# Kernel tuning notes

Measured on AMD Instinct MI355X. Metric: run time of the kernel, lower is better.

Reference implementation:

```python
import jax, jax.numpy as jnp
import numpy as np

EMB = 1024
HID = 4096
B = 2
T = 4096
NUM_BLOCK = 24
EPS = 1e-6


def rmsnorm(x):
    # unparameterized RMS normalization over last dim
    return x * jax.lax.rsqrt(jnp.mean(jnp.square(x), axis=-1, keepdims=True) + EPS)


def setup_inputs() -> dict:
    key = jax.random.key(0)
    k1, k2, k3, k4 = jax.random.split(key, 4)
    x = jax.random.normal(k1, (B, T, EMB), dtype=jnp.float32)
    W1 = 0.02 * jax.random.normal(k2, (HID, EMB), dtype=jnp.float32)
    W2 = 0.02 * jax.random.normal(k3, (HID, EMB), dtype=jnp.float32)
    W3 = (0.02 / np.sqrt(NUM_BLOCK)) * jax.random.normal(k4, (EMB, HID), dtype=jnp.float32)
    return {"x": x, "W1": W1, "W2": W2, "W3": W3}


def bar_quadratic_causal_preact_stable(a, b):
    # y_t = (1/t^2) * sum_{i<=t} sum_{j<=t} exp(a_i + b_j), per feature channel.
    # exp factorizes, so compute stably via log-cumsum-exp along the seq axis.
    seq = a.shape[1]
    log_t = jnp.log(jnp.arange(1, seq + 1, dtype=a.dtype))  # [T]
    la = jax.lax.cumlogsumexp(a, axis=1)  # [B,T,H]
    lb = jax.lax.cumlogsumexp(b, axis=1)  # [B,T,H]
    return jnp.exp(la + lb - 2.0 * log_t[None, :, None])


def reference(x, W1, W2, W3):
    r = rmsnorm(x)
    a = jnp.einsum('bte,he->bth', r, W1)  # fc_1, no bias
    b = jnp.einsum('bte,he->bth', r, W2)  # fc_2, no bias
    r = bar_quadratic_causal_preact_stable(a, b)
    r = rmsnorm(r)
    r = jnp.einsum('bth,eh->bte', r, W3)  # fc_3, no bias
    return x + r
```

## Files before the change

kernel.cpp:

```cpp
#include <hip/hip_runtime.h>
#include <hip/hip_fp8.h>

#define EMB 1024
#define HID 4096
#define NB 2
#define TT 4096
#define MROWS (NB*TT)
#define N1 (2*HID)
#define CHUNK 128
#define NCH 32

typedef short short8 __attribute__((ext_vector_type(8)));
typedef float v4f   __attribute__((ext_vector_type(4)));
typedef int   v4i   __attribute__((ext_vector_type(4)));
typedef int   v8i   __attribute__((ext_vector_type(8)));

__device__ __forceinline__ unsigned short f2bf(float f) {
  unsigned int u = __float_as_uint(f);
  u += 0x7FFFu + ((u >> 16) & 1u);
  return (unsigned short)(u >> 16);
}
__device__ __forceinline__ float bf2f(unsigned short s) {
  return __uint_as_float(((unsigned int)s) << 16);
}
__device__ __forceinline__ unsigned char f2e4m3(float f) {
  __hip_fp8_e4m3 q(f);
  return *(unsigned char*)&q;
}
__device__ __forceinline__ float e4m32f(unsigned char c) {
  __hip_fp8_e4m3 q = *(__hip_fp8_e4m3*)&c;
  return (float)q;
}
__device__ __forceinline__ void g2l16(const void* g, void* l) {
  __builtin_amdgcn_global_load_lds(
      (const __attribute__((address_space(1))) void*)g,
      (__attribute__((address_space(3))) void*)l, 16, 0, 0);
}

__device__ __forceinline__ float block_reduce_sum(float v, float* sbuf) {
  #pragma unroll
  for (int off = 32; off; off >>= 1) v += __shfl_down(v, off, 64);
  int lane = threadIdx.x & 63, w = threadIdx.x >> 6;
  if (lane == 0) sbuf[w] = v;
  __syncthreads();
  return sbuf[0] + sbuf[1] + sbuf[2] + sbuf[3];
}

__global__ __launch_bounds__(256) void conv_all(const float* __restrict__ W1,
                                                const float* __restrict__ W2,
                                                const float* __restrict__ W3,
                                                unsigned short* __restrict__ o12,
                                                unsigned char* __restrict__ o3) {
  size_t i = ((size_t)blockIdx.x*256 + threadIdx.x)*4;
  if (i < 2ull*HID*EMB) {
    const float* s = (i < (size_t)HID*EMB) ? (W1 + i) : (W2 + (i - (size_t)HID*EMB));
    float4 v = *(const float4*)s;
    ushort4 u; u.x=f2bf(v.x); u.y=f2bf(v.y); u.z=f2bf(v.z); u.w=f2bf(v.w);
    *(ushort4*)(o12 + i) = u;
  } else {
    size_t off = i - 2ull*HID*EMB;
    float4 v = *(const float4*)(W3 + off);
    uchar4 u; u.x=f2e4m3(v.x*64.f); u.y=f2e4m3(v.y*64.f);
             u.z=f2e4m3(v.z*64.f); u.w=f2e4m3(v.w*64.f);
    *(uchar4*)(o3 + off) = u;
  }
}

__global__ __launch_bounds__(256) void rmsnorm_x(const float* __restrict__ x,
                                                 unsigned short* __restrict__ r) {
  __shared__ float sbuf[4];
  int row = blockIdx.x;
  float4 v = *(const float4*)(x + (size_t)row*EMB + threadIdx.x*4);
  float ss = v.x*v.x + v.y*v.y + v.z*v.z + v.w*v.w;
  float tot = block_reduce_sum(ss, sbuf);
  float sc = rsqrtf(tot * (1.0f/EMB) + 1e-6f);
  ushort4 o; o.x=f2bf(v.x*sc); o.y=f2bf(v.y*sc); o.z=f2bf(v.z*sc); o.w=f2bf(v.w*sc);
  *(ushort4*)(r + (size_t)row*EMB + threadIdx.x*4) = o;
}

__global__ __launch_bounds__(256, 2)
void gemm_exp(const unsigned short* __restrict__ A,
              const unsigned short* __restrict__ Bt,
              unsigned char* __restrict__ C8,
              float* __restrict__ part,
              int K, int N) {
  __shared__ short lA[128*64];
  __shared__ short lB[128*64];
  const int tid  = threadIdx.x;
  const int lane = tid & 63;
  const int wm   = (tid >> 6) >> 1, wn = (tid >> 6) & 1;
  const int bid  = blockIdx.x;
  const int s0i  = bid >> 3;
  const int rowTile = s0i >> 3;
  const int colTile = ((bid & 7) << 3) | (s0i & 7);
  const int rowBase = rowTile * 128;
  const int colBase = colTile * 128;

  v4f acc[4][4];
  #pragma unroll
  for (int i=0;i<4;++i)
    #pragma unroll
    for (int j=0;j<4;++j) acc[i][j] = (v4f){0.f,0.f,0.f,0.f};

  for (int k0 = 0; k0 < K; k0 += 64) {
    #pragma unroll
    for (int j = 0; j < 4; ++j) {
      int s = j*256 + tid;
      int m = s >> 3;
      int c = (s & 7) ^ (m & 7);
      g2l16(A + (size_t)(rowBase + m)*K + k0 + c*8, &lA[s*8]);
    }
    #pragma unroll
    for (int j = 0; j < 4; ++j) {
      int s = j*256 + tid;
      int m = s >> 3;
      int c = (s & 7) ^ (m & 7);
      g2l16(Bt + (size_t)(colBase + m)*K + k0 + c*8, &lB[s*8]);
    }
    __syncthreads();
    #pragma unroll
    for (int s2 = 0; s2 < 2; ++s2) {
      const int quad = lane >> 4;
      const int cc = s2*4 + quad;
      short8 aF[4], bF[4];
      #pragma unroll
      for (int mt = 0; mt < 4; ++mt) {
        int ml = wm*64 + mt*16 + (lane & 15);
        aF[mt] = *(const short8*)&lA[(ml*8 + (cc ^ (ml & 7)))*8];
      }
      #pragma unroll
      for (int nt = 0; nt < 4; ++nt) {
        int nl = wn*64 + nt*16 + (lane & 15);
        bF[nt] = *(const short8*)&lB[(nl*8 + (cc ^ (nl & 7)))*8];
      }
      #pragma unroll
      for (int mt = 0; mt < 4; ++mt)
        #pragma unroll
        for (int nt = 0; nt < 4; ++nt)
          acc[mt][nt] = __builtin_amdgcn_mfma_f32_16x16x32_bf16(aF[mt], bF[nt], acc[mt][nt], 0, 0, 0);
    }
    __syncthreads();
  }

  const int quad = lane >> 4, c15 = lane & 15;
  float csum[4] = {0.f, 0.f, 0.f, 0.f};
  #pragma unroll
  for (int mt = 0; mt < 4; ++mt) {
    #pragma unroll
    for (int nt = 0; nt < 4; ++nt) {
      int col = colBase + wn*64 + nt*16 + c15;
      #pragma unroll
      for (int r = 0; r < 4; ++r) {
        int row = rowBase + wm*64 + mt*16 + quad*4 + r;
        size_t idx = (size_t)row*N + col;
        float e = __expf(acc[mt][nt][r]);
        C8[idx] = f2e4m3(e);
        csum[nt] += e;
      }
    }
  }
  float* cs = (float*)lA;
  #pragma unroll
  for (int nt = 0; nt < 4; ++nt) {
    float s = csum[nt];
    s += __shfl_xor(s, 16, 64);
    s += __shfl_xor(s, 32, 64);
    if (lane < 16) cs[wm*128 + wn*64 + nt*16 + lane] = s;
  }
  __syncthreads();
  if (tid < 128)
    part[(size_t)(colBase + tid)*64 + rowTile] = cs[tid] + cs[128 + tid];
}

__global__ __launch_bounds__(256, 2)
void gemm_out(const unsigned char* __restrict__ A8,
              const unsigned char* __restrict__ B8,
              const float* __restrict__ x,
              const float* __restrict__ rsq,
              float* __restrict__ out,
              int K, int N) {
  __shared__ unsigned char lA8[128*128];
  __shared__ unsigned char lB8[128*128];
  const int tid  = threadIdx.x;
  const int lane = tid & 63;
  const int wm   = (tid >> 6) >> 1, wn = (tid >> 6) & 1;
  const int rowBase = blockIdx.x * 128;
  const int colBase = blockIdx.y * 128;
  const int q   = lane >> 4;
  const int r15 = lane & 15;

  v4f acc[4][4];
  #pragma unroll
  for (int i=0;i<4;++i)
    #pragma unroll
    for (int j=0;j<4;++j) acc[i][j] = (v4f){0.f,0.f,0.f,0.f};

  for (int k0 = 0; k0 < K; k0 += 128) {
    #pragma unroll
    for (int j = 0; j < 4; ++j) {
      int s = j*256 + tid;
      int m = s >> 3;
      int c = (s & 7) ^ (m & 7);
      g2l16(A8 + (size_t)(rowBase + m)*K + k0 + c*16, &lA8[s*16]);
    }
    #pragma unroll
    for (int j = 0; j < 4; ++j) {
      int s = j*256 + tid;
      int m = s >> 3;
      int c = (s & 7) ^ (m & 7);
      g2l16(B8 + (size_t)(colBase + m)*K + k0 + c*16, &lB8[s*16]);
    }
    __syncthreads();
    v8i aF[4], bF[4];
    #pragma unroll
    for (int mt = 0; mt < 4; ++mt) {
      int ml = wm*64 + mt*16 + r15;
      int s  = ml & 7;
      v4i lo = *(const v4i*)&lA8[ml*128 + (((2*q)   ^ s)<<4)];
      v4i hi = *(const v4i*)&lA8[ml*128 + (((2*q+1) ^ s)<<4)];
      aF[mt] = __builtin_shufflevector(lo, hi, 0,1,2,3,4,5,6,7);
    }
    #pragma unroll
    for (int nt = 0; nt < 4; ++nt) {
      int nl = wn*64 + nt*16 + r15;
      int s  = nl & 7;
      v4i lo = *(const v4i*)&lB8[nl*128 + (((2*q)   ^ s)<<4)];
      v4i hi = *(const v4i*)&lB8[nl*128 + (((2*q+1) ^ s)<<4)];
      bF[nt] = __builtin_shufflevector(lo, hi, 0,1,2,3,4,5,6,7);
    }
    #pragma unroll
    for (int mt = 0; mt < 4; ++mt)
      #pragma unroll
      for (int nt = 0; nt < 4; ++nt)
        acc[mt][nt] = __builtin_amdgcn_mfma_scale_f32_16x16x128_f8f6f4(
            aF[mt], bF[nt], acc[mt][nt],
            0, 0,
            0, 0x7F7F7F7F,
            0, 0x7F7F7F7F);
    __syncthreads();
  }

  const int quad = lane >> 4, c15 = lane & 15;
  #pragma unroll
  for (int mt = 0; mt < 4; ++mt) {
    #pragma unroll
    for (int nt = 0; nt < 4; ++nt) {
      int col = colBase + wn*64 + nt*16 + c15;
      #pragma unroll
      for (int r = 0; r < 4; ++r) {
        int row = rowBase + wm*64 + mt*16 + quad*4 + r;
        size_t idx = (size_t)row*N + col;
        float sc = rsqrtf(rsq[row]*(1.0f/HID) + 1e-6f) * 0.0625f;
        out[idx] = x[idx] + sc*acc[mt][nt][r];
      }
    }
  }
}

__global__ __launch_bounds__(256) void scan_prefix(float* __restrict__ part,
                                                   float* __restrict__ rsq) {
  int idx = blockIdx.x*256 + threadIdx.x;
  if (idx < MROWS) rsq[idx] = 0.f;
  int col = idx >> 1, bb = idx & 1;
  float* p = part + (size_t)col*64 + bb*NCH;
  float run = 0.f;
  #pragma unroll
  for (int c = 0; c < NCH; ++c) { float v = p[c]; p[c] = run; run += v; }
}

__global__ __launch_bounds__(256) void scan_emit(const unsigned char* __restrict__ ab,
                                                 const float* __restrict__ part,
                                                 unsigned char* __restrict__ y8,
                                                 float* __restrict__ rsq) {
  int h = blockIdx.x*256 + threadIdx.x;
  int cy = blockIdx.y, bb = blockIdx.z;
  int lane = threadIdx.x & 63;
  float sa = part[(size_t)h*64 + bb*NCH + cy];
  float sb = part[(size_t)(HID + h)*64 + bb*NCH + cy];
  const unsigned char* pa = ab + ((size_t)(bb*TT + cy*CHUNK))*N1 + h;
  const unsigned char* pb = pa + HID;
  unsigned char* py = y8 + ((size_t)(bb*TT + cy*CHUNK))*HID + h;
  float* prs = rsq + bb*TT + cy*CHUNK;
  int t0 = cy*CHUNK;
  #pragma unroll 4
  for (int i = 0; i < CHUNK; ++i) {
    sa += e4m32f(pa[(size_t)i*N1]);
    sb += e4m32f(pb[(size_t)i*N1]);
    float inv = __builtin_amdgcn_rcpf((float)(t0 + i + 1));
    float y = sa*sb*inv*inv;
    py[(size_t)i*HID] = f2e4m3(y*0.25f);
    float s2 = y*y;
    #pragma unroll
    for (int off = 32; off; off >>= 1) s2 += __shfl_xor(s2, off, 64);
    if (lane == 0) atomicAdd(&prs[i], s2);
  }
}

extern "C" void kernel_launch(void* const* d_in, const int* in_sizes, int n_in,
                              void* d_out, int out_size, void* d_ws, size_t ws_size,
                              hipStream_t stream) {
  const float* x  = (const float*)d_in[0];
  const float* W1 = (const float*)d_in[1];
  const float* W2 = (const float*)d_in[2];
  const float* W3 = (const float*)d_in[3];
  float* out = (float*)d_out;
  char* ws = (char*)d_ws;

  unsigned short* r_bf   = (unsigned short*)(ws);
  unsigned short* w12_bf = (unsigned short*)(ws + 16777216ull);
  unsigned char*  w3_8   = (unsigned char*) (ws + 33554432ull);
  unsigned char*  ab8    = (unsigned char*) (ws + 37748736ull);
  float*          rsq    = (float*)        (ws + 104857600ull);
  unsigned char*  y8     = (unsigned char*) (ws + 171966464ull);
  float*          part   = (float*)d_out;

  conv_all<<<12288, 256, 0, stream>>>(W1, W2, W3, w12_bf, w3_8);
  rmsnorm_x<<<MROWS, 256, 0, stream>>>(x, r_bf);
  gemm_exp<<<4096, 256, 0, stream>>>(r_bf, w12_bf, ab8, part, EMB, N1);
  scan_prefix<<<64, 256, 0, stream>>>(part, rsq);
  scan_emit<<<dim3(16,NCH,2), 256, 0, stream>>>(ab8, part, y8, rsq);
  gemm_out<<<dim3(64,8), 256, 0, stream>>>(y8, w3_8, x, rsq, out, HID, EMB);
}
```

Before: 406.8 us.

## Replace per-timestep atomic row sums with separate fp8 row-sum-of-squares kernel

The scan kernel no longer does a wavefront shuffle reduction and an atomicAdd per timestep to build per-row sums of squares. A new rowss kernel recomputes them from the quantized fp8 output, and the scale constant changes to match the 0.25-prescaled values. The scan now handles four channels per thread with uchar4 loads and stores and a deeper unroll, and gemm_out hoists the per-row scale out of the inner column loop. The cost is an extra launch plus a re-read of y8, and the norm is now computed from quantized values instead of full-precision ones.

```diff
diff --git a/kernel.cpp b/kernel.cpp
--- a/kernel.cpp
+++ b/kernel.cpp
@@ -243,6 +243,12 @@
   const int quad = lane >> 4, c15 = lane & 15;
   #pragma unroll
   for (int mt = 0; mt < 4; ++mt) {
+    float scr[4];
+    #pragma unroll
+    for (int r = 0; r < 4; ++r) {
+      int row = rowBase + wm*64 + mt*16 + quad*4 + r;
+      scr[r] = rsqrtf(rsq[row]*(1.0f/256.0f) + 1e-6f) * 0.0625f;
+    }
     #pragma unroll
     for (int nt = 0; nt < 4; ++nt) {
       int col = colBase + wn*64 + nt*16 + c15;
@@ -250,17 +256,14 @@
       for (int r = 0; r < 4; ++r) {
         int row = rowBase + wm*64 + mt*16 + quad*4 + r;
         size_t idx = (size_t)row*N + col;
-        float sc = rsqrtf(rsq[row]*(1.0f/HID) + 1e-6f) * 0.0625f;
-        out[idx] = x[idx] + sc*acc[mt][nt][r];
+        out[idx] = x[idx] + scr[r]*acc[mt][nt][r];
       }
     }
   }
 }
 
-__global__ __launch_bounds__(256) void scan_prefix(float* __restrict__ part,
-                                                   float* __restrict__ rsq) {
+__global__ __launch_bounds__(256) void scan_prefix(float* __restrict__ part) {
   int idx = blockIdx.x*256 + threadIdx.x;
-  if (idx < MROWS) rsq[idx] = 0.f;
   int col = idx >> 1, bb = idx & 1;
   float* p = part + (size_t)col*64 + bb*NCH;
   float run = 0.f;
@@ -270,30 +273,53 @@
 
 __global__ __launch_bounds__(256) void scan_emit(const unsigned char* __restrict__ ab,
                                                  const float* __restrict__ part,
-                                                 unsigned char* __restrict__ y8,
-                                                 float* __restrict__ rsq) {
-  int h = blockIdx.x*256 + threadIdx.x;
+                                                 unsigned char* __restrict__ y8) {
+  int h0 = (blockIdx.x*256 + threadIdx.x)*4;
   int cy = blockIdx.y, bb = blockIdx.z;
-  int lane = threadIdx.x & 63;
-  float sa = part[(size_t)h*64 + bb*NCH + cy];
-  float sb = part[(size_t)(HID + h)*64 + bb*NCH + cy];
-  const unsigned char* pa = ab + ((size_t)(bb*TT + cy*CHUNK))*N1 + h;
+  float sa[4], sb[4];
+  #pragma unroll
+  for (int j = 0; j < 4; ++j) {
+    sa[j] = part[(size_t)(h0+j)*64 + bb*NCH + cy];
+    sb[j] = part[(size_t)(HID + h0+j)*64 + bb*NCH + cy];
+  }
+  const unsigned char* pa = ab + ((size_t)(bb*TT + cy*CHUNK))*N1 + h0;
   const unsigned char* pb = pa + HID;
-  unsigned char* py = y8 + ((size_t)(bb*TT + cy*CHUNK))*HID + h;
-  float* prs = rsq + bb*TT + cy*CHUNK;
+  unsigned char* py = y8 + ((size_t)(bb*TT + cy*CHUNK))*HID + h0;
   int t0 = cy*CHUNK;
-  #pragma unroll 4
+  #pragma unroll 8
   for (int i = 0; i < CHUNK; ++i) {
-    sa += e4m32f(pa[(size_t)i*N1]);
-    sb += e4m32f(pb[(size_t)i*N1]);
+    uchar4 va = *(const uchar4*)(pa + (size_t)i*N1);
+    uchar4 vb = *(const uchar4*)(pb + (size_t)i*N1);
+    sa[0] += e4m32f(va.x); sa[1] += e4m32f(va.y);
+    sa[2] += e4m32f(va.z); sa[3] += e4m32f(va.w);
+    sb[0] += e4m32f(vb.x); sb[1] += e4m32f(vb.y);
+    sb[2] += e4m32f(vb.z); sb[3] += e4m32f(vb.w);
     float inv = __builtin_amdgcn_rcpf((float)(t0 + i + 1));
-    float y = sa*sb*inv*inv;
-    py[(size_t)i*HID] = f2e4m3(y*0.25f);
-    float s2 = y*y;
-    #pragma unroll
-    for (int off = 32; off; off >>= 1) s2 += __shfl_xor(s2, off, 64);
-    if (lane == 0) atomicAdd(&prs[i], s2);
-  }
+    float i2 = inv*inv*0.25f;
+    uchar4 o;
+    o.x = f2e4m3(sa[0]*sb[0]*i2); o.y = f2e4m3(sa[1]*sb[1]*i2);
+    o.z = f2e4m3(sa[2]*sb[2]*i2); o.w = f2e4m3(sa[3]*sb[3]*i2);
+    *(uchar4*)(py + (size_t)i*HID) = o;
+  }
+}
+
+__global__ __launch_bounds__(256) void rowss(const unsigned char* __restrict__ y8,
+                                             float* __restrict__ rsq) {
+  __shared__ float sbuf[4];
+  int row = blockIdx.x;
+  const unsigned char* p = y8 + (size_t)row*HID + threadIdx.x*16;
+  uint4 v = *(const uint4*)p;
+  float ss = 0.f;
+  unsigned int w[4] = {v.x, v.y, v.z, v.w};
+  #pragma unroll
+  for (int g = 0; g < 4; ++g)
+    #pragma unroll
+    for (int b = 0; b < 4; ++b) {
+      float f = e4m32f((unsigned char)(w[g] >> (8*b)));
+      ss += f*f;
+    }
+  float tot = block_reduce_sum(ss, sbuf);
+  if (threadIdx.x == 0) rsq[row] = tot;
 }
 
 extern "C" void kernel_launch(void* const* d_in, const int* in_sizes, int n_in,
@@ -317,7 +343,8 @@
   conv_all<<<12288, 256, 0, stream>>>(W1, W2, W3, w12_bf, w3_8);
   rmsnorm_x<<<MROWS, 256, 0, stream>>>(x, r_bf);
   gemm_exp<<<4096, 256, 0, stream>>>(r_bf, w12_bf, ab8, part, EMB, N1);
-  scan_prefix<<<64, 256, 0, stream>>>(part, rsq);
-  scan_emit<<<dim3(16,NCH,2), 256, 0, stream>>>(ab8, part, y8, rsq);
+  scan_prefix<<<64, 256, 0, stream>>>(part);
+  scan_emit<<<dim3(4,NCH,2), 256, 0, stream>>>(ab8, part, y8);
+  rowss<<<MROWS, 256, 0, stream>>>(y8, rsq);
   gemm_out<<<dim3(64,8), 256, 0, stream>>>(y8, w3_8, x, rsq, out, HID, EMB);
 }
```

Result: faster. 335.8 us (-17.5%).
